# Kernel tuning notes

Measured on AMD Instinct MI355X. Metric: run time of the kernel, lower is better.

## Reference

```python
import jax, jax.numpy as jnp
import numpy as np

NUM_EXPERTS = 64
TOP_K = 2
CAPACITY_FACTOR = 1.25
D_MODEL = 2048
BATCH, SEQ = 4, 4096


def setup_inputs() -> dict:
    key = jax.random.key(0)
    kx, kw = jax.random.split(key)
    x = jax.random.normal(kx, (BATCH, SEQ, D_MODEL), dtype=jnp.float32)
    # router weight: Linear(input_dim, num_experts, bias=False), init std=0.001
    W = jax.random.normal(kw, (NUM_EXPERTS, D_MODEL), dtype=jnp.float32) * 0.001
    return {"x": x, "W": W}


def reference(x, W):
    B, S, D = x.shape
    N = B * S  # combined batch of tokens
    E = NUM_EXPERTS
    k = TOP_K
    capacity = int(CAPACITY_FACTOR * N * k / E)  # static Python int

    x_flat = x.reshape(N, D)
    router_logits = jnp.einsum('nd,ed->ne', x_flat, W)  # [N, E]
    routing_weights = jax.nn.softmax(router_logits, axis=-1)

    top_k_weights, top_k_indices = jax.lax.top_k(routing_weights, k)  # [N, k]
    top_k_weights = top_k_weights / (top_k_weights.sum(-1, keepdims=True) + 1e-8)

    expert_counts = jnp.zeros((E,), dtype=jnp.float32)
    dispatch_mask = jnp.zeros((N, E), dtype=jnp.float32)
    token_ids = jnp.arange(N)

    # Sequential over k (fixed, small): within a k-step the capacity check uses
    # counts from previous steps only, matching the torch scatter semantics.
    for k_idx in range(k):
        expert_idx = top_k_indices[:, k_idx]            # [N]
        under_cap = expert_counts[expert_idx] < capacity  # [N] bool
        expert_counts = expert_counts + jax.ops.segment_sum(
            under_cap.astype(jnp.float32), expert_idx, num_segments=E)
        # top-k experts are distinct per token, so add == set on zero-init slots
        dispatch_mask = dispatch_mask.at[token_ids, expert_idx].add(
            jnp.where(under_cap, top_k_weights[:, k_idx], 0.0))

    # Tokens that got dropped everywhere go to the least-loaded expert with w=1
    unrouted = dispatch_mask.sum(-1) == 0                     # [N]
    least_loaded = jnp.argmax(capacity - expert_counts)       # scalar
    dispatch_mask = jnp.where(
        unrouted[:, None] & (jnp.arange(E)[None, :] == least_loaded),
        1.0, dispatch_mask)

    normalized_dispatch_mask = dispatch_mask / (dispatch_mask.sum(-1, keepdims=True) + 1e-8)

    router_z_loss = jnp.mean(jnp.square(router_logits))
    counts = normalized_dispatch_mask.sum(0)                  # [E]
    target_count = float(N * k / E)
    load_balance_loss = jnp.mean(jnp.square(counts / float(N) - target_count / float(N)))
    router_loss = 0.001 * jax.lax.stop_gradient(router_z_loss) \
                + 0.001 * jax.lax.stop_gradient(load_balance_loss)

    return (jax.lax.stop_gradient(routing_weights), normalized_dispatch_mask, router_loss)
```

## Files before the change

kernel.cpp:

```cpp
#include <hip/hip_runtime.h>
#include <math.h>

#define N_TOK 16384
#define D_MODEL 2048
#define N_EXP 64
#define CAPACITY 640
#define NREP 8

#define BK 64
#define NSTAGE (D_MODEL / BK)
#define LPW 72

typedef __attribute__((ext_vector_type(8))) _Float16 h8;
typedef __attribute__((ext_vector_type(4))) float f4;

__global__ __launch_bounds__(256) void k0_cvtw(const float* __restrict__ W,
                                               _Float16* __restrict__ WHg,
                                               _Float16* __restrict__ WLg) {
  const int i = (blockIdx.x * 256 + threadIdx.x) * 8;
  const float4 a = *(const float4*)(W + i);
  const float4 b = *(const float4*)(W + i + 4);
  const float f[8] = {a.x, a.y, a.z, a.w, b.x, b.y, b.z, b.w};
  h8 hh, ll;
#pragma unroll
  for (int j = 0; j < 8; j++) {
    const float s = f[j] * 1024.f;
    const _Float16 h = (_Float16)s;
    hh[j] = h;
    ll[j] = (_Float16)((s - (float)h) * 1024.f);
  }
  *(h8*)(WHg + i) = hh;
  *(h8*)(WLg + i) = ll;
}

__global__ __launch_bounds__(256, 2) void k12_gemm_softmax(
    const float* __restrict__ x, const _Float16* __restrict__ WHg,
    const _Float16* __restrict__ WLg, float* __restrict__ rw_out,
    int2* __restrict__ top12, float2* __restrict__ wts,
    int* __restrict__ histR, float* __restrict__ zR) {
  __shared__ __align__(16) _Float16 WHs[2][64][LPW];
  __shared__ __align__(16) _Float16 WLs[2][64][LPW];
  __shared__ float slog[32][65];
  __shared__ float zred[4];

  const int t = threadIdx.x;
  const int lane = t & 63;
  const int wid = t >> 6;
  const int wm = wid >> 1;
  const int wn = wid & 1;
  const int m0 = blockIdx.x * 32;
  const int rep = blockIdx.x & (NREP - 1);

  const int we = t >> 2;
  const int wcc = (t & 3) * 16;
  const int frow = lane & 15;
  const int fk = (lane >> 4) * 8;

  const _Float16* whg = WHg + (size_t)we * D_MODEL + wcc;
  const _Float16* wlg = WLg + (size_t)we * D_MODEL + wcc;
  const float* xg = x + (size_t)(m0 + wm * 16 + frow) * D_MODEL + fk;

  h8 wh[2][2], wl[2][2];
  float4 xreg[2][4];
  h8 afh[2][2], afl[2][2];
  f4 acc1[2], acc2[2];
#pragma unroll
  for (int i = 0; i < 2; i++) {
    acc1[i] = (f4)(0.f);
    acc2[i] = (f4)(0.f);
  }

#define LOAD_W(slot, s)                             \
  {                                                 \
    const _Float16* ph_ = whg + (s) * BK;           \
    const _Float16* pl_ = wlg + (s) * BK;           \
    wh[slot][0] = *(const h8*)(ph_);                \
    wh[slot][1] = *(const h8*)(ph_ + 8);            \
    wl[slot][0] = *(const h8*)(pl_);                \
    wl[slot][1] = *(const h8*)(pl_ + 8);            \
  }
#define LOAD_X(slot, s)                        \
  {                                            \
    const float* p_ = xg + (s) * BK;           \
    xreg[slot][0] = *(const float4*)(p_);      \
    xreg[slot][1] = *(const float4*)(p_ + 4);  \
    xreg[slot][2] = *(const float4*)(p_ + 32); \
    xreg[slot][3] = *(const float4*)(p_ + 36); \
  }
#define STORE_W(slot, buf)                     \
  {                                            \
    *(h8*)&WHs[buf][we][wcc] = wh[slot][0];    \
    *(h8*)&WHs[buf][we][wcc + 8] = wh[slot][1]; \
    *(h8*)&WLs[buf][we][wcc] = wl[slot][0];    \
    *(h8*)&WLs[buf][we][wcc + 8] = wl[slot][1]; \
  }
#define CVT_X(slot)                                                    \
  {                                                                    \
    float xf[16] = {xreg[slot][0].x, xreg[slot][0].y, xreg[slot][0].z, \
                    xreg[slot][0].w, xreg[slot][1].x, xreg[slot][1].y, \
                    xreg[slot][1].z, xreg[slot][1].w, xreg[slot][2].x, \
                    xreg[slot][2].y, xreg[slot][2].z, xreg[slot][2].w, \
                    xreg[slot][3].x, xreg[slot][3].y, xreg[slot][3].z, \
                    xreg[slot][3].w};                                  \
    _Pragma("unroll") for (int j = 0; j < 8; j++) {                    \
      _Float16 a_ = (_Float16)xf[j];                                   \
      afh[slot][0][j] = a_;                                            \
      afl[slot][0][j] = (_Float16)((xf[j] - (float)a_) * 1024.f);      \
      _Float16 b_ = (_Float16)xf[j + 8];                               \
      afh[slot][1][j] = b_;                                            \
      afl[slot][1][j] = (_Float16)((xf[j + 8] - (float)b_) * 1024.f);  \
    }                                                                  \
  }
#define COMPUTE(buf, p)                                                       \
  {                                                                           \
    _Pragma("unroll") for (int ks = 0; ks < 2; ks++) {                        \
      _Pragma("unroll") for (int nt = 0; nt < 2; nt++) {                      \
        h8 bh = *(const h8*)&WHs[buf][wn * 32 + nt * 16 + frow][ks * 32 + fk]; \
        h8 bl = *(const h8*)&WLs[buf][wn * 32 + nt * 16 + frow][ks * 32 + fk]; \
        acc1[nt] = __builtin_amdgcn_mfma_f32_16x16x32_f16(afh[p][ks], bh,     \
                                                          acc1[nt], 0, 0, 0);  \
        acc2[nt] = __builtin_amdgcn_mfma_f32_16x16x32_f16(afl[p][ks], bh,     \
                                                          acc2[nt], 0, 0, 0);  \
        acc2[nt] = __builtin_amdgcn_mfma_f32_16x16x32_f16(afh[p][ks], bl,     \
                                                          acc2[nt], 0, 0, 0);  \
      }                                                                       \
    }                                                                         \
  }
#define PHASE(p, s)                 \
  {                                 \
    if ((s) + 1 < NSTAGE) {         \
      STORE_W(1 - (p), 1 - (p));    \
      CVT_X(1 - (p));               \
    }                               \
    if ((s) + 3 < NSTAGE) {         \
      LOAD_W(1 - (p), (s) + 3);     \
      LOAD_X(1 - (p), (s) + 3);     \
    }                               \
    COMPUTE((p), (p));              \
    __syncthreads();                \
  }

  LOAD_W(0, 0);
  LOAD_X(0, 0);
  LOAD_W(1, 1);
  LOAD_X(1, 1);
  STORE_W(0, 0);
  CVT_X(0);
  LOAD_W(0, 2);
  LOAD_X(0, 2);
  __syncthreads();

  for (int it = 0; it < NSTAGE; it += 2) {
    PHASE(0, it);
    PHASE(1, it + 1);
  }

  const int cg = lane >> 4, ci = lane & 15;
#pragma unroll
  for (int nt = 0; nt < 2; nt++)
#pragma unroll
    for (int r = 0; r < 4; r++) {
      const float v =
          (acc1[nt][r] + acc2[nt][r] * 0.0009765625f) * 0.0009765625f;
      slog[wm * 16 + cg * 4 + r][wn * 32 + nt * 16 + ci] = v;
    }
  __syncthreads();

  float z_acc = 0.f;
  for (int tt = 0; tt < 8; tt++) {
    const int tloc = wid * 8 + tt;
    const int n = m0 + tloc;
    const float v = slog[tloc][lane];
    z_acc += v * v;
    float mx = v;
#pragma unroll
    for (int off = 32; off; off >>= 1) mx = fmaxf(mx, __shfl_xor(mx, off));
    const float p = __expf(v - mx);
    float ssum = p;
#pragma unroll
    for (int off = 32; off; off >>= 1) ssum += __shfl_xor(ssum, off);
    const float rw = p / ssum;
    rw_out[(size_t)n * N_EXP + lane] = rw;

    const unsigned long long b1 = __ballot(v == mx);
    const int i1 = __builtin_ctzll(b1);
    float v2 = (lane == i1) ? -INFINITY : v;
#pragma unroll
    for (int off = 32; off; off >>= 1) v2 = fmaxf(v2, __shfl_xor(v2, off));
    const unsigned long long b2 = __ballot(v == v2) & ~(1ull << i1);
    const int i2 = __builtin_ctzll(b2);
    const float rw1 = __shfl(rw, i1);
    const float rw2 = __shfl(rw, i2);
    if (lane == 0) {
      const float denom = rw1 + rw2 + 1e-8f;
      top12[n] = make_int2(i1, i2);
      wts[n] = make_float2(rw1 / denom, rw2 / denom);
      atomicAdd(&histR[(rep * N_EXP + i1) * 16], 1);
    }
  }
#pragma unroll
  for (int off = 32; off; off >>= 1) z_acc += __shfl_xor(z_acc, off);
  if (lane == 0) zred[wid] = z_acc;
  __syncthreads();
  if (t == 0) atomicAdd(&zR[rep * 16], zred[0] + zred[1] + zred[2] + zred[3]);
}

__global__ __launch_bounds__(256) void k3_dispatch(
    const int2* __restrict__ top12, const float2* __restrict__ wts,
    const int* __restrict__ histR, float* __restrict__ mask_out,
    float* __restrict__ cntR) {
  const int lane = threadIdx.x & 63;
  const int wid = threadIdx.x >> 6;
  const int n = blockIdx.x * 4 + wid;
  const int rep = blockIdx.x & (NREP - 1);

  const int2 ij = top12[n];
  const float2 w = wts[n];
  int h = 0;
#pragma unroll
  for (int r = 0; r < NREP; r++) h += histR[(r * N_EXP + ij.y) * 16];
  const bool allowed = h < CAPACITY;
  const float ssum = w.x + (allowed ? w.y : 0.f);
  const float inv = 1.f / (ssum + 1e-8f);
  float val = 0.f;
  if (lane == ij.x) val = w.x * inv;
  else if (allowed && lane == ij.y) val = w.y * inv;
  mask_out[(size_t)n * N_EXP + lane] = val;
  if (val != 0.f) atomicAdd(&cntR[(rep * N_EXP + lane) * 16], val);
}

__global__ void k4_loss(const float* __restrict__ cntR,
                        const float* __restrict__ zR,
                        float* __restrict__ loss_out) {
  const int lane = threadIdx.x;
  float c = 0.f;
#pragma unroll
  for (int r = 0; r < NREP; r++) c += cntR[(r * N_EXP + lane) * 16];
  const float d = (c - 512.0f) * (1.0f / 16384.0f);
  float v = d * d;
#pragma unroll
  for (int off = 32; off; off >>= 1) v += __shfl_xor(v, off);
  if (lane == 0) {
    float z = 0.f;
#pragma unroll
    for (int r = 0; r < NREP; r++) z += zR[r * 16];
    const float lb = v * (1.0f / 64.0f);
    loss_out[0] = 0.001f * (z * (1.0f / (16384.0f * 64.0f))) + 0.001f * lb;
  }
}

extern "C" void kernel_launch(void* const* d_in, const int* in_sizes, int n_in,
                              void* d_out, int out_size, void* d_ws,
                              size_t ws_size, hipStream_t stream) {
  const float* x = (const float*)d_in[0];
  const float* W = (const float*)d_in[1];
  float* out = (float*)d_out;
  float* rw_out = out;
  float* mask_out = out + (size_t)N_TOK * N_EXP;
  float* loss_out = out + 2 * (size_t)N_TOK * N_EXP;

  char* ws = (char*)d_ws;
  int* histR = (int*)ws;
  float* cntR = (float*)(ws + 32768);
  float* zR = (float*)(ws + 65536);
  int2* top12 = (int2*)(ws + 131072);
  float2* wts = (float2*)(ws + 262144);
  _Float16* WHg = (_Float16*)(ws + 393216);
  _Float16* WLg = (_Float16*)(ws + 655360);

  hipMemsetAsync(histR, 0, 65536 + 512, stream);
  k0_cvtw<<<64, 256, 0, stream>>>(W, WHg, WLg);
  k12_gemm_softmax<<<512, 256, 0, stream>>>(x, WHg, WLg, rw_out, top12, wts,
                                            histR, zR);
  k3_dispatch<<<N_TOK / 4, 256, 0, stream>>>(top12, wts, histR, mask_out,
                                             cntR);
  k4_loss<<<1, 64, 0, stream>>>(cntR, zR, loss_out);
}
```

Before: 222.5 us.

## Split router GEMM block across 8 waves with 16-expert slices each

```diff
diff --git a/kernel.cpp b/kernel.cpp
--- a/kernel.cpp
+++ b/kernel.cpp
@@ -33,7 +33,7 @@
   *(h8*)(WLg + i) = ll;
 }
 
-__global__ __launch_bounds__(256, 2) void k12_gemm_softmax(
+__global__ __launch_bounds__(512, 4) void k12_gemm_softmax(
     const float* __restrict__ x, const _Float16* __restrict__ WHg,
     const _Float16* __restrict__ WLg, float* __restrict__ rw_out,
     int2* __restrict__ top12, float2* __restrict__ wts,
@@ -41,18 +41,18 @@
   __shared__ __align__(16) _Float16 WHs[2][64][LPW];
   __shared__ __align__(16) _Float16 WLs[2][64][LPW];
   __shared__ float slog[32][65];
-  __shared__ float zred[4];
+  __shared__ float zred[8];
 
   const int t = threadIdx.x;
   const int lane = t & 63;
   const int wid = t >> 6;
-  const int wm = wid >> 1;
-  const int wn = wid & 1;
+  const int wm = wid >> 2;
+  const int wn = wid & 3;
   const int m0 = blockIdx.x * 32;
   const int rep = blockIdx.x & (NREP - 1);
 
-  const int we = t >> 2;
-  const int wcc = (t & 3) * 16;
+  const int we = t >> 3;
+  const int wcc = (t & 7) * 8;
   const int frow = lane & 15;
   const int fk = (lane >> 4) * 8;
 
@@ -60,24 +60,15 @@
   const _Float16* wlg = WLg + (size_t)we * D_MODEL + wcc;
   const float* xg = x + (size_t)(m0 + wm * 16 + frow) * D_MODEL + fk;
 
-  h8 wh[2][2], wl[2][2];
+  h8 wh[2], wl[2];
   float4 xreg[2][4];
   h8 afh[2][2], afl[2][2];
-  f4 acc1[2], acc2[2];
-#pragma unroll
-  for (int i = 0; i < 2; i++) {
-    acc1[i] = (f4)(0.f);
-    acc2[i] = (f4)(0.f);
-  }
-
-#define LOAD_W(slot, s)                             \
-  {                                                 \
-    const _Float16* ph_ = whg + (s) * BK;           \
-    const _Float16* pl_ = wlg + (s) * BK;           \
-    wh[slot][0] = *(const h8*)(ph_);                \
-    wh[slot][1] = *(const h8*)(ph_ + 8);            \
-    wl[slot][0] = *(const h8*)(pl_);                \
-    wl[slot][1] = *(const h8*)(pl_ + 8);            \
+  f4 acc1 = (f4)(0.f), acc2 = (f4)(0.f);
+
+#define LOAD_W(slot, s)                      \
+  {                                          \
+    wh[slot] = *(const h8*)(whg + (s) * BK); \
+    wl[slot] = *(const h8*)(wlg + (s) * BK); \
   }
 #define LOAD_X(slot, s)                        \
   {                                            \
@@ -87,12 +78,10 @@
     xreg[slot][2] = *(const float4*)(p_ + 32); \
     xreg[slot][3] = *(const float4*)(p_ + 36); \
   }
-#define STORE_W(slot, buf)                     \
-  {                                            \
-    *(h8*)&WHs[buf][we][wcc] = wh[slot][0];    \
-    *(h8*)&WHs[buf][we][wcc + 8] = wh[slot][1]; \
-    *(h8*)&WLs[buf][we][wcc] = wl[slot][0];    \
-    *(h8*)&WLs[buf][we][wcc + 8] = wl[slot][1]; \
+#define STORE_W(slot, buf)                \
+  {                                       \
+    *(h8*)&WHs[buf][we][wcc] = wh[slot];  \
+    *(h8*)&WLs[buf][we][wcc] = wl[slot];  \
   }
 #define CVT_X(slot)                                                    \
   {                                                                    \
@@ -111,33 +100,31 @@
       afl[slot][1][j] = (_Float16)((xf[j + 8] - (float)b_) * 1024.f);  \
     }                                                                  \
   }
-#define COMPUTE(buf, p)                                                       \
-  {                                                                           \
-    _Pragma("unroll") for (int ks = 0; ks < 2; ks++) {                        \
-      _Pragma("unroll") for (int nt = 0; nt < 2; nt++) {                      \
-        h8 bh = *(const h8*)&WHs[buf][wn * 32 + nt * 16 + frow][ks * 32 + fk]; \
-        h8 bl = *(const h8*)&WLs[buf][wn * 32 + nt * 16 + frow][ks * 32 + fk]; \
-        acc1[nt] = __builtin_amdgcn_mfma_f32_16x16x32_f16(afh[p][ks], bh,     \
-                                                          acc1[nt], 0, 0, 0);  \
-        acc2[nt] = __builtin_amdgcn_mfma_f32_16x16x32_f16(afl[p][ks], bh,     \
-                                                          acc2[nt], 0, 0, 0);  \
-        acc2[nt] = __builtin_amdgcn_mfma_f32_16x16x32_f16(afh[p][ks], bl,     \
-                                                          acc2[nt], 0, 0, 0);  \
-      }                                                                       \
-    }                                                                         \
-  }
-#define PHASE(p, s)                 \
-  {                                 \
-    if ((s) + 1 < NSTAGE) {         \
-      STORE_W(1 - (p), 1 - (p));    \
-      CVT_X(1 - (p));               \
-    }                               \
-    if ((s) + 3 < NSTAGE) {         \
-      LOAD_W(1 - (p), (s) + 3);     \
-      LOAD_X(1 - (p), (s) + 3);     \
-    }                               \
-    COMPUTE((p), (p));              \
-    __syncthreads();                \
+#define COMPUTE(buf, p)                                                   \
+  {                                                                       \
+    _Pragma("unroll") for (int ks = 0; ks < 2; ks++) {                    \
+      h8 bh = *(const h8*)&WHs[buf][wn * 16 + frow][ks * 32 + fk];        \
+      h8 bl = *(const h8*)&WLs[buf][wn * 16 + frow][ks * 32 + fk];        \
+      acc1 = __builtin_amdgcn_mfma_f32_16x16x32_f16(afh[p][ks], bh, acc1, \
+                                                    0, 0, 0);             \
+      acc2 = __builtin_amdgcn_mfma_f32_16x16x32_f16(afl[p][ks], bh, acc2, \
+                                                    0, 0, 0);             \
+      acc2 = __builtin_amdgcn_mfma_f32_16x16x32_f16(afh[p][ks], bl, acc2, \
+                                                    0, 0, 0);             \
+    }                                                                     \
+  }
+#define PHASE(p, s)              \
+  {                              \
+    if ((s) + 1 < NSTAGE) {      \
+      STORE_W(1 - (p), 1 - (p)); \
+      CVT_X(1 - (p));            \
+    }                            \
+    if ((s) + 3 < NSTAGE) {      \
+      LOAD_W(1 - (p), (s) + 3);  \
+      LOAD_X(1 - (p), (s) + 3);  \
+    }                            \
+    COMPUTE((p), (p));           \
+    __syncthreads();             \
   }
 
   LOAD_W(0, 0);
@@ -157,18 +144,15 @@
 
   const int cg = lane >> 4, ci = lane & 15;
 #pragma unroll
-  for (int nt = 0; nt < 2; nt++)
-#pragma unroll
-    for (int r = 0; r < 4; r++) {
-      const float v =
-          (acc1[nt][r] + acc2[nt][r] * 0.0009765625f) * 0.0009765625f;
-      slog[wm * 16 + cg * 4 + r][wn * 32 + nt * 16 + ci] = v;
-    }
+  for (int r = 0; r < 4; r++) {
+    const float v = (acc1[r] + acc2[r] * 0.0009765625f) * 0.0009765625f;
+    slog[wm * 16 + cg * 4 + r][wn * 16 + ci] = v;
+  }
   __syncthreads();
 
   float z_acc = 0.f;
-  for (int tt = 0; tt < 8; tt++) {
-    const int tloc = wid * 8 + tt;
+  for (int tt = 0; tt < 4; tt++) {
+    const int tloc = wid * 4 + tt;
     const int n = m0 + tloc;
     const float v = slog[tloc][lane];
     z_acc += v * v;
@@ -202,7 +186,12 @@
   for (int off = 32; off; off >>= 1) z_acc += __shfl_xor(z_acc, off);
   if (lane == 0) zred[wid] = z_acc;
   __syncthreads();
-  if (t == 0) atomicAdd(&zR[rep * 16], zred[0] + zred[1] + zred[2] + zred[3]);
+  if (t == 0) {
+    float zs = 0.f;
+#pragma unroll
+    for (int i = 0; i < 8; i++) zs += zred[i];
+    atomicAdd(&zR[rep * 16], zs);
+  }
 }
 
 __global__ __launch_bounds__(256) void k3_dispatch(
@@ -270,7 +259,7 @@
 
   hipMemsetAsync(histR, 0, 65536 + 512, stream);
   k0_cvtw<<<64, 256, 0, stream>>>(W, WHg, WLg);
-  k12_gemm_softmax<<<512, 256, 0, stream>>>(x, WHg, WLg, rw_out, top12, wts,
+  k12_gemm_softmax<<<512, 512, 0, stream>>>(x, WHg, WLg, rw_out, top12, wts,
                                             histR, zR);
   k3_dispatch<<<N_TOK / 4, 256, 0, stream>>>(top12, wts, histR, mask_out,
                                              cntR);
```

After: 230.9 us. 3.8% more time.

## Pre-swizzle W into MFMA fragment layout and drop LDS staging in router GEMM

Applied to the files above, without the earlier changes.

```diff
diff --git a/kernel.cpp b/kernel.cpp
--- a/kernel.cpp
+++ b/kernel.cpp
@@ -6,20 +6,22 @@
 #define N_EXP 64
 #define CAPACITY 640
 #define NREP 8
-
-#define BK 64
-#define NSTAGE (D_MODEL / BK)
-#define LPW 72
+#define NS 64
 
 typedef __attribute__((ext_vector_type(8))) _Float16 h8;
 typedef __attribute__((ext_vector_type(4))) float f4;
 
 __global__ __launch_bounds__(256) void k0_cvtw(const float* __restrict__ W,
-                                               _Float16* __restrict__ WHg,
-                                               _Float16* __restrict__ WLg) {
-  const int i = (blockIdx.x * 256 + threadIdx.x) * 8;
-  const float4 a = *(const float4*)(W + i);
-  const float4 b = *(const float4*)(W + i + 4);
+                                               _Float16* __restrict__ WTH,
+                                               _Float16* __restrict__ WTL) {
+  const int t = threadIdx.x;
+  const int lane = t & 63;
+  const int c = blockIdx.x * 4 + (t >> 6);
+  const int e = (c & 3) * 16 + (lane & 15);
+  const int k = (c >> 2) * 32 + (lane >> 4) * 8;
+  const float* src = W + (size_t)e * D_MODEL + k;
+  const float4 a = *(const float4*)src;
+  const float4 b = *(const float4*)(src + 4);
   const float f[8] = {a.x, a.y, a.z, a.w, b.x, b.y, b.z, b.w};
   h8 hh, ll;
 #pragma unroll
@@ -29,40 +31,33 @@
     hh[j] = h;
     ll[j] = (_Float16)((s - (float)h) * 1024.f);
   }
-  *(h8*)(WHg + i) = hh;
-  *(h8*)(WLg + i) = ll;
-}
-
-__global__ __launch_bounds__(256, 2) void k12_gemm_softmax(
-    const float* __restrict__ x, const _Float16* __restrict__ WHg,
-    const _Float16* __restrict__ WLg, float* __restrict__ rw_out,
+  *(h8*)(WTH + c * 512 + lane * 8) = hh;
+  *(h8*)(WTL + c * 512 + lane * 8) = ll;
+}
+
+__global__ __launch_bounds__(128, 4) void k12_gemm_softmax(
+    const float* __restrict__ x, const _Float16* __restrict__ WTH,
+    const _Float16* __restrict__ WTL, float* __restrict__ rw_out,
     int2* __restrict__ top12, float2* __restrict__ wts,
     int* __restrict__ histR, float* __restrict__ zR) {
-  __shared__ __align__(16) _Float16 WHs[2][64][LPW];
-  __shared__ __align__(16) _Float16 WLs[2][64][LPW];
-  __shared__ float slog[32][65];
-  __shared__ float zred[4];
+  __shared__ float slog[16][65];
+  __shared__ float zred[2];
 
   const int t = threadIdx.x;
   const int lane = t & 63;
-  const int wid = t >> 6;
-  const int wm = wid >> 1;
-  const int wn = wid & 1;
-  const int m0 = blockIdx.x * 32;
+  const int wn = t >> 6;
+  const int m0 = blockIdx.x * 16;
   const int rep = blockIdx.x & (NREP - 1);
 
-  const int we = t >> 2;
-  const int wcc = (t & 3) * 16;
   const int frow = lane & 15;
   const int fk = (lane >> 4) * 8;
 
-  const _Float16* whg = WHg + (size_t)we * D_MODEL + wcc;
-  const _Float16* wlg = WLg + (size_t)we * D_MODEL + wcc;
-  const float* xg = x + (size_t)(m0 + wm * 16 + frow) * D_MODEL + fk;
-
-  h8 wh[2][2], wl[2][2];
-  float4 xreg[2][4];
-  h8 afh[2][2], afl[2][2];
+  const float* xg = x + (size_t)(m0 + frow) * D_MODEL + fk;
+  const _Float16* wth = WTH + (wn * 2) * 512 + lane * 8;
+  const _Float16* wtl = WTL + (wn * 2) * 512 + lane * 8;
+
+  float4 xr[4][2];
+  h8 wh_[2][2], wl_[2][2];
   f4 acc1[2], acc2[2];
 #pragma unroll
   for (int i = 0; i < 2; i++) {
@@ -70,89 +65,58 @@
     acc2[i] = (f4)(0.f);
   }
 
-#define LOAD_W(slot, s)                             \
-  {                                                 \
-    const _Float16* ph_ = whg + (s) * BK;           \
-    const _Float16* pl_ = wlg + (s) * BK;           \
-    wh[slot][0] = *(const h8*)(ph_);                \
-    wh[slot][1] = *(const h8*)(ph_ + 8);            \
-    wl[slot][0] = *(const h8*)(pl_);                \
-    wl[slot][1] = *(const h8*)(pl_ + 8);            \
-  }
-#define LOAD_X(slot, s)                        \
+#define LX(sl, s)                          \
+  {                                        \
+    const float* p_ = xg + (s) * 32;       \
+    xr[sl][0] = *(const float4*)p_;        \
+    xr[sl][1] = *(const float4*)(p_ + 4);  \
+  }
+#define LW(sl, s)                              \
   {                                            \
-    const float* p_ = xg + (s) * BK;           \
-    xreg[slot][0] = *(const float4*)(p_);      \
-    xreg[slot][1] = *(const float4*)(p_ + 4);  \
-    xreg[slot][2] = *(const float4*)(p_ + 32); \
-    xreg[slot][3] = *(const float4*)(p_ + 36); \
-  }
-#define STORE_W(slot, buf)                     \
-  {                                            \
-    *(h8*)&WHs[buf][we][wcc] = wh[slot][0];    \
-    *(h8*)&WHs[buf][we][wcc + 8] = wh[slot][1]; \
-    *(h8*)&WLs[buf][we][wcc] = wl[slot][0];    \
-    *(h8*)&WLs[buf][we][wcc + 8] = wl[slot][1]; \
-  }
-#define CVT_X(slot)                                                    \
-  {                                                                    \
-    float xf[16] = {xreg[slot][0].x, xreg[slot][0].y, xreg[slot][0].z, \
-                    xreg[slot][0].w, xreg[slot][1].x, xreg[slot][1].y, \
-                    xreg[slot][1].z, xreg[slot][1].w, xreg[slot][2].x, \
-                    xreg[slot][2].y, xreg[slot][2].z, xreg[slot][2].w, \
-                    xreg[slot][3].x, xreg[slot][3].y, xreg[slot][3].z, \
-                    xreg[slot][3].w};                                  \
-    _Pragma("unroll") for (int j = 0; j < 8; j++) {                    \
-      _Float16 a_ = (_Float16)xf[j];                                   \
-      afh[slot][0][j] = a_;                                            \
-      afl[slot][0][j] = (_Float16)((xf[j] - (float)a_) * 1024.f);      \
-      _Float16 b_ = (_Float16)xf[j + 8];                               \
-      afh[slot][1][j] = b_;                                            \
-      afl[slot][1][j] = (_Float16)((xf[j + 8] - (float)b_) * 1024.f);  \
-    }                                                                  \
-  }
-#define COMPUTE(buf, p)                                                       \
-  {                                                                           \
-    _Pragma("unroll") for (int ks = 0; ks < 2; ks++) {                        \
-      _Pragma("unroll") for (int nt = 0; nt < 2; nt++) {                      \
-        h8 bh = *(const h8*)&WHs[buf][wn * 32 + nt * 16 + frow][ks * 32 + fk]; \
-        h8 bl = *(const h8*)&WLs[buf][wn * 32 + nt * 16 + frow][ks * 32 + fk]; \
-        acc1[nt] = __builtin_amdgcn_mfma_f32_16x16x32_f16(afh[p][ks], bh,     \
-                                                          acc1[nt], 0, 0, 0);  \
-        acc2[nt] = __builtin_amdgcn_mfma_f32_16x16x32_f16(afl[p][ks], bh,     \
-                                                          acc2[nt], 0, 0, 0);  \
-        acc2[nt] = __builtin_amdgcn_mfma_f32_16x16x32_f16(afh[p][ks], bl,     \
-                                                          acc2[nt], 0, 0, 0);  \
-      }                                                                       \
-    }                                                                         \
-  }
-#define PHASE(p, s)                 \
-  {                                 \
-    if ((s) + 1 < NSTAGE) {         \
-      STORE_W(1 - (p), 1 - (p));    \
-      CVT_X(1 - (p));               \
-    }                               \
-    if ((s) + 3 < NSTAGE) {         \
-      LOAD_W(1 - (p), (s) + 3);     \
-      LOAD_X(1 - (p), (s) + 3);     \
-    }                               \
-    COMPUTE((p), (p));              \
-    __syncthreads();                \
-  }
-
-  LOAD_W(0, 0);
-  LOAD_X(0, 0);
-  LOAD_W(1, 1);
-  LOAD_X(1, 1);
-  STORE_W(0, 0);
-  CVT_X(0);
-  LOAD_W(0, 2);
-  LOAD_X(0, 2);
-  __syncthreads();
-
-  for (int it = 0; it < NSTAGE; it += 2) {
-    PHASE(0, it);
-    PHASE(1, it + 1);
+    const _Float16* ph_ = wth + (s) * 2048;    \
+    const _Float16* pl_ = wtl + (s) * 2048;    \
+    wh_[sl][0] = *(const h8*)ph_;              \
+    wh_[sl][1] = *(const h8*)(ph_ + 512);      \
+    wl_[sl][0] = *(const h8*)pl_;              \
+    wl_[sl][1] = *(const h8*)(pl_ + 512);      \
+  }
+#define STEP(xs, ws, s)                                                     \
+  {                                                                         \
+    h8 ah, al;                                                              \
+    {                                                                       \
+      const float xf[8] = {xr[xs][0].x, xr[xs][0].y, xr[xs][0].z,           \
+                           xr[xs][0].w, xr[xs][1].x, xr[xs][1].y,           \
+                           xr[xs][1].z, xr[xs][1].w};                       \
+      _Pragma("unroll") for (int j = 0; j < 8; j++) {                       \
+        const _Float16 a_ = (_Float16)xf[j];                                \
+        ah[j] = a_;                                                         \
+        al[j] = (_Float16)((xf[j] - (float)a_) * 1024.f);                   \
+      }                                                                     \
+    }                                                                       \
+    _Pragma("unroll") for (int nt = 0; nt < 2; nt++) {                      \
+      acc1[nt] = __builtin_amdgcn_mfma_f32_16x16x32_f16(ah, wh_[ws][nt],    \
+                                                        acc1[nt], 0, 0, 0); \
+      acc2[nt] = __builtin_amdgcn_mfma_f32_16x16x32_f16(al, wh_[ws][nt],    \
+                                                        acc2[nt], 0, 0, 0); \
+      acc2[nt] = __builtin_amdgcn_mfma_f32_16x16x32_f16(ah, wl_[ws][nt],    \
+                                                        acc2[nt], 0, 0, 0); \
+    }                                                                       \
+    if ((s) + 2 < NS) LW(ws, (s) + 2);                                      \
+    if ((s) + 4 < NS) LX(xs, (s) + 4);                                      \
+  }
+
+  LX(0, 0);
+  LX(1, 1);
+  LX(2, 2);
+  LX(3, 3);
+  LW(0, 0);
+  LW(1, 1);
+
+  for (int g = 0; g < NS; g += 4) {
+    STEP(0, 0, g);
+    STEP(1, 1, g + 1);
+    STEP(2, 0, g + 2);
+    STEP(3, 1, g + 3);
   }
 
   const int cg = lane >> 4, ci = lane & 15;
@@ -162,13 +126,13 @@
     for (int r = 0; r < 4; r++) {
       const float v =
           (acc1[nt][r] + acc2[nt][r] * 0.0009765625f) * 0.0009765625f;
-      slog[wm * 16 + cg * 4 + r][wn * 32 + nt * 16 + ci] = v;
+      slog[cg * 4 + r][wn * 32 + nt * 16 + ci] = v;
     }
   __syncthreads();
 
   float z_acc = 0.f;
   for (int tt = 0; tt < 8; tt++) {
-    const int tloc = wid * 8 + tt;
+    const int tloc = wn * 8 + tt;
     const int n = m0 + tloc;
     const float v = slog[tloc][lane];
     z_acc += v * v;
@@ -200,9 +164,9 @@
   }
 #pragma unroll
   for (int off = 32; off; off >>= 1) z_acc += __shfl_xor(z_acc, off);
-  if (lane == 0) zred[wid] = z_acc;
+  if (lane == 0) zred[wn] = z_acc;
   __syncthreads();
-  if (t == 0) atomicAdd(&zR[rep * 16], zred[0] + zred[1] + zred[2] + zred[3]);
+  if (t == 0) atomicAdd(&zR[rep * 16], zred[0] + zred[1]);
 }
 
 __global__ __launch_bounds__(256) void k3_dispatch(
@@ -265,13 +229,13 @@
   float* zR = (float*)(ws + 65536);
   int2* top12 = (int2*)(ws + 131072);
   float2* wts = (float2*)(ws + 262144);
-  _Float16* WHg = (_Float16*)(ws + 393216);
-  _Float16* WLg = (_Float16*)(ws + 655360);
+  _Float16* WTH = (_Float16*)(ws + 393216);
+  _Float16* WTL = (_Float16*)(ws + 655360);
 
   hipMemsetAsync(histR, 0, 65536 + 512, stream);
-  k0_cvtw<<<64, 256, 0, stream>>>(W, WHg, WLg);
-  k12_gemm_softmax<<<512, 256, 0, stream>>>(x, WHg, WLg, rw_out, top12, wts,
-                                            histR, zR);
+  k0_cvtw<<<64, 256, 0, stream>>>(W, WTH, WTL);
+  k12_gemm_softmax<<<1024, 128, 0, stream>>>(x, WTH, WTL, rw_out, top12, wts,
+                                             histR, zR);
   k3_dispatch<<<N_TOK / 4, 256, 0, stream>>>(top12, wts, histR, mask_out,
                                              cntR);
   k4_loss<<<1, 64, 0, stream>>>(cntR, zR, loss_out);
```

After: 229.7 us. 3.2% more time.
